# Performance work log

Measured on AMD Instinct MI355X. Metric: run time of the kernel, lower is better.

Reference implementation:

```python
import jax, jax.numpy as jnp
import numpy as np

B, D_IN = 4096, 1024
E, K = 16, 2
EMB = 256
H1, H2 = 2048, 1024  # hidden_units, hidden_units // 2
O = 512              # num_classes


def setup_inputs() -> dict:
    key = jax.random.key(0)
    ks = jax.random.split(key, 10)
    s = lambda *sh: 1.0 / np.sqrt(sh[-2] if len(sh) > 1 else 1.0)
    return {
        "x":   jax.random.normal(ks[0], (B, D_IN), jnp.float32),
        "Wr":  jax.random.normal(ks[1], (D_IN, EMB), jnp.float32) * (1.0 / np.sqrt(D_IN)),
        "br":  jnp.zeros((EMB,), jnp.float32),
        "emb": jax.random.normal(ks[2], (E, EMB), jnp.float32) * (1.0 / np.sqrt(EMB)),
        "W1":  jax.random.normal(ks[3], (E, D_IN, H1), jnp.float32) * (1.0 / np.sqrt(D_IN)),
        "b1":  jnp.zeros((E, H1), jnp.float32),
        "W2":  jax.random.normal(ks[4], (E, H1, H2), jnp.float32) * (1.0 / np.sqrt(H1)),
        "b2":  jnp.zeros((E, H2), jnp.float32),
        "W3":  jax.random.normal(ks[5], (E, H2, O), jnp.float32) * (1.0 / np.sqrt(H2)),
        "b3":  jnp.zeros((E, O), jnp.float32),
    }


def reference(x, Wr, br, emb, W1, b1, W2, b2, W3, b3):
    # Router query: [B, EMB]
    q = x @ Wr + br
    # Negative squared euclidean distance to expert embeddings -> scores [B, E]
    d2 = jnp.sum(jnp.square(q[:, None, :] - emb[None, :, :]), axis=-1)
    scores = -d2
    gating_probs = jax.nn.softmax(scores, axis=-1)  # [B, E]
    # Top-k selection + renormalized gates
    top_v, top_i = jax.lax.top_k(scores, K)          # [B, K]
    gates = jax.nn.softmax(top_v, axis=-1)           # [B, K]
    # All experts run on full batch (dense), batched over expert axis
    h1 = jax.nn.relu(jnp.einsum('bi,eih->beh', x, W1) + b1)   # [B, E, H1]
    h2 = jax.nn.relu(jnp.einsum('beh,ehm->bem', h1, W2) + b2)  # [B, E, H2]
    out = jnp.einsum('bem,emo->beo', h2, W3) + b3              # [B, E, O]
    # Gather top-k expert outputs per example and combine
    sel = jnp.take_along_axis(out, top_i[:, :, None], axis=1)  # [B, K, O]
    final = jnp.sum(sel * gates[:, :, None], axis=1)           # [B, O]
    return final, q, gating_probs
```

## Files before the change

### kernel.cpp

```cpp
#include <hip/hip_runtime.h>
#include <hip/hip_bf16.h>

using bf16 = __hip_bfloat16;
typedef __attribute__((ext_vector_type(8))) short bf16x8;
typedef __attribute__((ext_vector_type(8))) unsigned short u16x8;
typedef __attribute__((ext_vector_type(4))) float f32x4;

constexpr int BATCH = 4096;
constexpr int D_IN  = 1024;
constexpr int NEXP  = 16;
constexpr int EMB   = 256;
constexpr int H1    = 2048;
constexpr int H2    = 1024;
constexpr int OUTD  = 512;
constexpr int SLOTS = BATCH * 2;
constexpr int SLOTS_PAD = SLOTS + 256;
constexpr int MAX_T256 = SLOTS / 256 + NEXP;
constexpr int MAX_T128 = SLOTS / 128 + NEXP;
constexpr int K3    = 3 * D_IN;

constexpr size_t WS_XB     = 0;
constexpr size_t WS_XLO    = WS_XB     + (size_t)BATCH * D_IN * 2;
constexpr size_t WS_H1     = WS_XLO    + (size_t)BATCH * D_IN * 2;
constexpr size_t WS_H2     = WS_H1     + (size_t)SLOTS_PAD * H1 * 2;
constexpr size_t WS_OSL    = WS_H2     + (size_t)SLOTS_PAD * H2 * 2;
constexpr size_t WS_TOPI   = WS_OSL    + (size_t)SLOTS_PAD * OUTD * 4;
constexpr size_t WS_GATES  = WS_TOPI   + (size_t)SLOTS * 4;
constexpr size_t WS_SLOTOF = WS_GATES  + (size_t)SLOTS * 4;
constexpr size_t WS_TOKL   = WS_SLOTOF + (size_t)SLOTS * 4;
constexpr size_t WS_CNT    = WS_TOKL   + (size_t)SLOTS_PAD * 4;
constexpr size_t WS_TMAP256= WS_CNT    + 64 * 4;
constexpr size_t WS_TMAP128= WS_TMAP256+ (size_t)MAX_T256 * 8;
constexpr size_t WS_WR3    = ((WS_TMAP128 + (size_t)MAX_T128 * 8) + 255) & ~(size_t)255;
constexpr size_t WS_WT     = ((WS_WR3 + (size_t)EMB * K3 * 2) + 255) & ~(size_t)255;

__device__ __forceinline__ unsigned short f2bf(float f) {
    bf16 h = __float2bfloat16(f);
    return __builtin_bit_cast(unsigned short, h);
}
__device__ __forceinline__ float bf2f(unsigned short h) {
    return __builtin_bit_cast(float, (unsigned)h << 16);
}

__device__ __forceinline__ void gload16(const unsigned short* g, unsigned short* l) {
    __builtin_amdgcn_global_load_lds(
        (const __attribute__((address_space(1))) unsigned int*)g,
        (__attribute__((address_space(3))) unsigned int*)l, 16, 0, 0);
}

template <int N>
__device__ __forceinline__ void waitcnt_vm() {
    static_assert(N == 0 || N == 4 || N == 8, "add case");
    if constexpr (N == 0) asm volatile("s_waitcnt vmcnt(0)" ::: "memory");
    else if constexpr (N == 4) asm volatile("s_waitcnt vmcnt(4)" ::: "memory");
    else if constexpr (N == 8) asm volatile("s_waitcnt vmcnt(8)" ::: "memory");
}

__global__ __launch_bounds__(256) void k_cvt_x(const float* __restrict__ x,
                                               unsigned short* __restrict__ xhi,
                                               unsigned short* __restrict__ xlo) {
    int i = blockIdx.x * 256 + threadIdx.x;
    float4 v = reinterpret_cast<const float4*>(x)[i];
    ushort4 h, l;
    h.x = f2bf(v.x); h.y = f2bf(v.y); h.z = f2bf(v.z); h.w = f2bf(v.w);
    l.x = f2bf(v.x - bf2f(h.x)); l.y = f2bf(v.y - bf2f(h.y));
    l.z = f2bf(v.z - bf2f(h.z)); l.w = f2bf(v.w - bf2f(h.w));
    reinterpret_cast<ushort4*>(xhi)[i] = h;
    reinterpret_cast<ushort4*>(xlo)[i] = l;
}

__global__ __launch_bounds__(256) void k_wr3(const float* __restrict__ Wr,
                                             unsigned short* __restrict__ Wrt3) {
    __shared__ float Tf[64][65];
    int n0 = blockIdx.x * 64, k0 = blockIdx.y * 64;
    const float* Wb = Wr + (size_t)k0 * EMB + n0;
    int t  = threadIdx.x;
    int kr = t >> 4, c4 = (t & 15) * 4;
#pragma unroll
    for (int i = 0; i < 4; i++) {
        float4 v = *reinterpret_cast<const float4*>(Wb + (size_t)(kr + i * 16) * EMB + c4);
        Tf[kr + i * 16][c4 + 0] = v.x; Tf[kr + i * 16][c4 + 1] = v.y;
        Tf[kr + i * 16][c4 + 2] = v.z; Tf[kr + i * 16][c4 + 3] = v.w;
    }
    __syncthreads();
#pragma unroll
    for (int i = 0; i < 2; i++) {
        int idx = t + i * 256;
        int n = idx >> 3, ck = (idx & 7) * 8;
        u16x8 hi, lo;
#pragma unroll
        for (int j = 0; j < 8; j++) {
            float w = Tf[ck + j][n];
            unsigned short h = f2bf(w);
            hi[j] = h; lo[j] = f2bf(w - bf2f(h));
        }
        unsigned short* dst = Wrt3 + (size_t)(n0 + n) * K3 + k0 + ck;
        *reinterpret_cast<u16x8*>(dst)            = hi;
        *reinterpret_cast<u16x8*>(dst + D_IN)     = hi;
        *reinterpret_cast<u16x8*>(dst + 2 * D_IN) = lo;
    }
}

__global__ __launch_bounds__(256) void k_wtrans(const float* __restrict__ W,
                                                unsigned short* __restrict__ Wt,
                                                int KD, int ND) {
    __shared__ float Tf[64][65];
    int e = blockIdx.z;
    int n0 = blockIdx.x * 64, k0 = blockIdx.y * 64;
    const float* Wb = W + ((size_t)e * KD + k0) * ND + n0;
    int t  = threadIdx.x;
    int kr = t >> 4, c4 = (t & 15) * 4;
#pragma unroll
    for (int i = 0; i < 4; i++) {
        float4 v = *reinterpret_cast<const float4*>(Wb + (size_t)(kr + i * 16) * ND + c4);
        Tf[kr + i * 16][c4 + 0] = v.x; Tf[kr + i * 16][c4 + 1] = v.y;
        Tf[kr + i * 16][c4 + 2] = v.z; Tf[kr + i * 16][c4 + 3] = v.w;
    }
    __syncthreads();
    unsigned short* Wtb = Wt + ((size_t)e * ND + n0) * KD + k0;
#pragma unroll
    for (int i = 0; i < 2; i++) {
        int idx = t + i * 256;
        int n = idx >> 3, ck = (idx & 7) * 8;
        u16x8 o;
#pragma unroll
        for (int j = 0; j < 8; j++) o[j] = f2bf(Tf[ck + j][n]);
        *reinterpret_cast<u16x8*>(Wtb + (size_t)n * KD + ck) = o;
    }
}

__global__ __launch_bounds__(256) void k_router3(const unsigned short* __restrict__ xhi,
                                                 const unsigned short* __restrict__ xlo,
                                                 const unsigned short* __restrict__ wrt3,
                                                 const float* __restrict__ br,
                                                 float* __restrict__ qout) {
    int nb = blockIdx.x * 64;
    int mb = blockIdx.y * 64;

    __shared__ __align__(16) unsigned short As[2][64 * 64];
    __shared__ __align__(16) unsigned short Bs[2][64 * 64];

    int t    = threadIdx.x;
    int lane = t & 63;
    int w    = t >> 6;
    int wr   = (w >> 1) * 32;
    int wc   = (w & 1) * 32;

    int srow = t >> 3;
    int swz  = (t & 7) ^ (srow & 7);
    size_t aoff[2], boff[2];
#pragma unroll
    for (int i = 0; i < 2; i++) {
        int row = i * 32 + srow;
        aoff[i] = (size_t)(mb + row) * D_IN + swz * 8;
        boff[i] = (size_t)(nb + row) * K3 + swz * 8;
    }

    auto STAGE = [&](int buf, int tts) {
        const unsigned short* abase = (tts >= 16 && tts < 32) ? xlo : xhi;
        int kk = (tts & 15) * 64;
#pragma unroll
        for (int i = 0; i < 2; i++) {
            gload16(abase + aoff[i] + kk, &As[buf][(i * 32 + w * 8) * 64] + lane * 8);
            gload16(wrt3 + boff[i] + tts * 64, &Bs[buf][(i * 32 + w * 8) * 64] + lane * 8);
        }
    };

    f32x4 acc[2][2];
#pragma unroll
    for (int mi = 0; mi < 2; mi++)
#pragma unroll
        for (int ni = 0; ni < 2; ni++) acc[mi][ni] = {0.f, 0.f, 0.f, 0.f};

    int lr  = lane & 15;
    int lkc = lane >> 4;

    constexpr int NT = K3 / 64;
    STAGE(0, 0);
    STAGE(1, 1);

    for (int tt = 0; tt < NT; tt++) {
        int cur = tt & 1;
        if (tt + 1 < NT) waitcnt_vm<4>(); else waitcnt_vm<0>();
        __builtin_amdgcn_s_barrier();
        const char* Ab = (const char*)As[cur];
        const char* Bb = (const char*)Bs[cur];
#pragma unroll
        for (int ks = 0; ks < 2; ks++) {
            bf16x8 a[2], b[2];
#pragma unroll
            for (int mi = 0; mi < 2; mi++) {
                int row = wr + mi * 16 + lr;
                int c   = (lkc + ks * 4) ^ (row & 7);
                a[mi] = *reinterpret_cast<const bf16x8*>(Ab + row * 128 + c * 16);
            }
#pragma unroll
            for (int ni = 0; ni < 2; ni++) {
                int row = wc + ni * 16 + lr;
                int c   = (lkc + ks * 4) ^ (row & 7);
                b[ni] = *reinterpret_cast<const bf16x8*>(Bb + row * 128 + c * 16);
            }
#pragma unroll
            for (int mi = 0; mi < 2; mi++)
#pragma unroll
                for (int ni = 0; ni < 2; ni++)
                    acc[mi][ni] = __builtin_amdgcn_mfma_f32_16x16x32_bf16(a[mi], b[ni], acc[mi][ni], 0, 0, 0);
        }
        __builtin_amdgcn_s_barrier();
        if (tt + 2 < NT) STAGE(cur, tt + 2);
    }

    int rowbase = (lane >> 4) * 4;
#pragma unroll
    for (int ni = 0; ni < 2; ni++) {
        int col = nb + wc + ni * 16 + lr;
        float bv = br[col];
#pragma unroll
        for (int mi = 0; mi < 2; mi++) {
#pragma unroll
            for (int qi = 0; qi < 4; qi++) {
                int row = mb + wr + mi * 16 + rowbase + qi;
                qout[(size_t)row * EMB + col] = acc[mi][ni][qi] + bv;
            }
        }
    }
}

__global__ __launch_bounds__(256) void k_router_topk(const float* __restrict__ q,
                                                     const float* __restrict__ emb,
                                                     float* __restrict__ gp,
                                                     int* __restrict__ topi,
                                                     float* __restrict__ gates) {
    int b    = blockIdx.x * 4 + (threadIdx.x >> 6);
    int lane = threadIdx.x & 63;
    int e    = lane & 15;
    int seg  = (lane >> 4) * 64;
    const float* qr = q + (size_t)b * EMB + seg;
    const float* er = emb + (size_t)e * EMB + seg;
    float d2 = 0.f;
#pragma unroll 8
    for (int i = 0; i < 64; i++) { float d = qr[i] - er[i]; d2 = fmaf(d, d, d2); }
    d2 += __shfl_xor(d2, 16);
    d2 += __shfl_xor(d2, 32);
    float s = -d2;
    float m = s;
#pragma unroll
    for (int o = 1; o < 16; o <<= 1) m = fmaxf(m, __shfl_xor(m, o));
    float ex  = __expf(s - m);
    float sum = ex;
#pragma unroll
    for (int o = 1; o < 16; o <<= 1) sum += __shfl_xor(sum, o);
    if (lane < 16) gp[(size_t)b * NEXP + lane] = ex / sum;
    float v1 = s; int i1 = e;
#pragma unroll
    for (int o = 1; o < 16; o <<= 1) {
        float ov = __shfl_xor(v1, o); int oi = __shfl_xor(i1, o);
        if (ov > v1 || (ov == v1 && oi < i1)) { v1 = ov; i1 = oi; }
    }
    float s2 = (e == i1) ? -1e30f : s;
    float v2 = s2; int i2 = e;
#pragma unroll
    for (int o = 1; o < 16; o <<= 1) {
        float ov = __shfl_xor(v2, o); int oi = __shfl_xor(i2, o);
        if (ov > v2 || (ov == v2 && oi < i2)) { v2 = ov; i2 = oi; }
    }
    if (lane == 0) {
        topi[b * 2] = i1; topi[b * 2 + 1] = i2;
        float tv  = __expf(v2 - v1);
        float inv = 1.f / (1.f + tv);
        gates[b * 2] = inv; gates[b * 2 + 1] = tv * inv;
    }
}

__global__ void k_zero(int* counts) { if (threadIdx.x < NEXP) counts[threadIdx.x] = 0; }

__global__ __launch_bounds__(256) void k_count(const int* __restrict__ topi, int* __restrict__ counts) {
    int i = blockIdx.x * 256 + threadIdx.x;
    atomicAdd(&counts[topi[i]], 1);
}

__global__ void k_scan(const int* __restrict__ counts, int* __restrict__ offsets,
                       int* __restrict__ cursors, int2* __restrict__ tmap256,
                       int2* __restrict__ tmap128) {
    if (threadIdx.x != 0) return;
    int off = 0;
    for (int e = 0; e < NEXP; e++) {
        offsets[e] = off; cursors[e] = off;
        off += counts[e];
    }
    for (int i = 0; i < MAX_T256; i++) tmap256[i] = make_int2(-1, 0);
    for (int i = 0; i < MAX_T128; i++) tmap128[i] = make_int2(-1, 0);
    {
        int binload[8] = {0, 0, 0, 0, 0, 0, 0, 0};
        for (int e = 0; e < NEXP; e++) {
            int rem = (counts[e] + 255) >> 8, ti = 0;
            while (rem > 0) {
                int b = 0;
                for (int q2 = 1; q2 < 8; q2++)
                    if (binload[q2] < binload[b]) b = q2;
                int space = 6 - binload[b];
                if (space <= 0) break;
                int take = (rem < space) ? rem : space;
                for (int i = 0; i < take; i++)
                    tmap256[b * 6 + binload[b] + i] = make_int2(e, (ti + i) * 256);
                binload[b] += take; ti += take; rem -= take;
            }
        }
    }
    {
        int binload[8] = {0, 0, 0, 0, 0, 0, 0, 0};
        for (int e = 0; e < NEXP; e++) {
            int rem = (counts[e] + 127) >> 7, ti = 0;
            while (rem > 0) {
                int b = 0;
                for (int q2 = 1; q2 < 8; q2++)
                    if (binload[q2] < binload[b]) b = q2;
                int space = 10 - binload[b];
                if (space <= 0) break;
                int take = (rem < space) ? rem : space;
                for (int i = 0; i < take; i++)
                    tmap128[b * 10 + binload[b] + i] = make_int2(e, (ti + i) * 128);
                binload[b] += take; ti += take; rem -= take;
            }
        }
    }
}

__global__ __launch_bounds__(256) void k_scatter(const int* __restrict__ topi, int* __restrict__ cursors,
                                                 int* __restrict__ toklist, int* __restrict__ slotof) {
    int i = blockIdx.x * 256 + threadIdx.x;
    int e = topi[i];
    int s = atomicAdd(&cursors[e], 1);
    toklist[s] = i >> 1;
    slotof[i]  = s;
}

template <int KD, int ND, int BM, int BN, int WM, int WN, int MODE, int MINW, int CAP>
__global__ __launch_bounds__(WM * WN * 64, MINW) void k_gemm(
    const unsigned short* __restrict__ Xin, const unsigned short* __restrict__ Wt,
    const float* __restrict__ bg, unsigned short* __restrict__ Hout,
    float* __restrict__ Oout, const int* __restrict__ counts,
    const int* __restrict__ offsets, const int* __restrict__ toklist,
    const int2* __restrict__ tmap) {
    constexpr int THREADS = WM * WN * 64;
    constexpr int FM = BM / (WM * 16);
    constexpr int FN = BN / (WN * 16);
    constexpr int A_ISS = BM * 8 / THREADS;
    constexpr int B_ISS = BN * 8 / THREADS;
    constexpr int RPI = THREADS / 8;
    constexpr int SL  = A_ISS + B_ISS;

    int id  = blockIdx.x;
    int bin = id & 7;
    int j   = id >> 3;
    int y   = bin * CAP + j % CAP;
    int xnb = j / CAP;

    int2 tm = tmap[y];
    int e = tm.x;
    if (e < 0) return;
    int base = tm.y;
    int n_e  = counts[e];
    int off  = offsets[e];
    int n0   = xnb * BN;

    __shared__ __align__(16) unsigned short As[2][BM * 64];
    __shared__ __align__(16) unsigned short Bs[2][BN * 64];

    int t    = threadIdx.x;
    int lane = t & 63;
    int w    = t >> 6;
    int wm   = w / WN;
    int wn   = w % WN;

    int srow  = t >> 3;
    int chunk = t & 7;
    const unsigned short* asrc[A_ISS];
    const unsigned short* bsrc[B_ISS];
#pragma unroll
    for (int i = 0; i < A_ISS; i++) {
        int row = i * RPI + srow;
        int swz = chunk ^ (row & 7);
        int g   = base + row;
        size_t arow;
        if (MODE == 0) {
            int gg = (g < n_e) ? g : (n_e - 1);
            arow = (size_t)toklist[off + gg];
        } else {
            arow = (size_t)(off + g);
        }
        asrc[i] = Xin + arow * KD + swz * 8;
    }
#pragma unroll
    for (int i = 0; i < B_ISS; i++) {
        int row = i * RPI + srow;
        int swz = chunk ^ (row & 7);
        bsrc[i] = Wt + ((size_t)e * ND + n0 + row) * KD + swz * 8;
    }

    auto STAGE = [&](int buf, int kt) {
#pragma unroll
        for (int i = 0; i < A_ISS; i++)
            gload16(asrc[i] + kt, &As[buf][(i * RPI + w * 8) * 64] + lane * 8);
#pragma unroll
        for (int i = 0; i < B_ISS; i++)
            gload16(bsrc[i] + kt, &Bs[buf][(i * RPI + w * 8) * 64] + lane * 8);
    };

    f32x4 acc[FM][FN];
#pragma unroll
    for (int mi = 0; mi < FM; mi++)
#pragma unroll
        for (int ni = 0; ni < FN; ni++) acc[mi][ni] = {0.f, 0.f, 0.f, 0.f};

    int lr  = lane & 15;
    int lkc = lane >> 4;

    constexpr int NT = KD / 64;
    STAGE(0, 0);
    STAGE(1, 64);

    for (int tt = 0; tt < NT; tt++) {
        int cur = tt & 1;
        if (tt + 1 < NT) waitcnt_vm<SL>(); else waitcnt_vm<0>();
        __builtin_amdgcn_s_barrier();
        const char* Ab = (const char*)As[cur];
        const char* Bb = (const char*)Bs[cur];
#pragma unroll
        for (int ks = 0; ks < 2; ks++) {
            bf16x8 b[FN];
#pragma unroll
            for (int ni = 0; ni < FN; ni++) {
                int row = wn * (BN / WN) + ni * 16 + lr;
                int c   = (lkc + ks * 4) ^ (row & 7);
                b[ni] = *reinterpret_cast<const bf16x8*>(Bb + row * 128 + c * 16);
            }
            bf16x8 a[FM];
#pragma unroll
            for (int mi = 0; mi < FM; mi++) {
                int row = wm * (BM / WM) + mi * 16 + lr;
                int c   = (lkc + ks * 4) ^ (row & 7);
                a[mi] = *reinterpret_cast<const bf16x8*>(Ab + row * 128 + c * 16);
            }
#pragma unroll
            for (int mi = 0; mi < FM; mi++)
#pragma unroll
                for (int ni = 0; ni < FN; ni++)
                    acc[mi][ni] = __builtin_amdgcn_mfma_f32_16x16x32_bf16(a[mi], b[ni], acc[mi][ni], 0, 0, 0);
        }
        __builtin_amdgcn_s_barrier();
        if (tt + 2 < NT) STAGE(cur, (tt + 2) * 64);
    }

    int rowbase = (lane >> 4) * 4;
#pragma unroll
    for (int ni = 0; ni < FN; ni++) {
        int col = n0 + wn * (BN / WN) + ni * 16 + lr;
        float bv = bg[(size_t)e * ND + col];
#pragma unroll
        for (int mi = 0; mi < FM; mi++) {
#pragma unroll
            for (int qi = 0; qi < 4; qi++) {
                int g = base + wm * (BM / WM) + mi * 16 + rowbase + qi;
                if (g < n_e) {
                    float v = acc[mi][ni][qi] + bv;
                    if (MODE == 2) {
                        Oout[(size_t)(off + g) * ND + col] = v;
                    } else {
                        v = fmaxf(v, 0.f);
                        Hout[(size_t)(off + g) * ND + col] = f2bf(v);
                    }
                }
            }
        }
    }
}

__global__ __launch_bounds__(128) void k_combine(const float* __restrict__ osl,
                                                 const float* __restrict__ gates,
                                                 const int* __restrict__ slotof,
                                                 float* __restrict__ outf) {
    int b = blockIdx.x;
    int j = threadIdx.x;
    int s0 = slotof[b * 2], s1 = slotof[b * 2 + 1];
    float g0 = gates[b * 2], g1 = gates[b * 2 + 1];
    float4 o0 = reinterpret_cast<const float4*>(osl + (size_t)s0 * OUTD)[j];
    float4 o1 = reinterpret_cast<const float4*>(osl + (size_t)s1 * OUTD)[j];
    float4 r;
    r.x = g0 * o0.x + g1 * o1.x;
    r.y = g0 * o0.y + g1 * o1.y;
    r.z = g0 * o0.z + g1 * o1.z;
    r.w = g0 * o0.w + g1 * o1.w;
    reinterpret_cast<float4*>(outf + (size_t)b * OUTD)[j] = r;
}

extern "C" void kernel_launch(void* const* d_in, const int* in_sizes, int n_in,
                              void* d_out, int out_size, void* d_ws, size_t ws_size,
                              hipStream_t stream) {
    const float* x   = (const float*)d_in[0];
    const float* Wr  = (const float*)d_in[1];
    const float* br  = (const float*)d_in[2];
    const float* emb = (const float*)d_in[3];
    const float* W1  = (const float*)d_in[4];
    const float* b1  = (const float*)d_in[5];
    const float* W2  = (const float*)d_in[6];
    const float* b2  = (const float*)d_in[7];
    const float* W3  = (const float*)d_in[8];
    const float* b3  = (const float*)d_in[9];

    float* out_final = (float*)d_out;
    float* out_q     = out_final + (size_t)BATCH * OUTD;
    float* out_gp    = out_q + (size_t)BATCH * EMB;

    char* ws = (char*)d_ws;
    unsigned short* xb  = (unsigned short*)(ws + WS_XB);
    unsigned short* xlo = (unsigned short*)(ws + WS_XLO);
    unsigned short* h1  = (unsigned short*)(ws + WS_H1);
    unsigned short* h2  = (unsigned short*)(ws + WS_H2);
    float* osl    = (float*)(ws + WS_OSL);
    int*   topi   = (int*)(ws + WS_TOPI);
    float* gates  = (float*)(ws + WS_GATES);
    int*   slotof = (int*)(ws + WS_SLOTOF);
    int*   toklist= (int*)(ws + WS_TOKL);
    int*   counts = (int*)(ws + WS_CNT);
    int*   offsets= counts + 16;
    int*   cursors= counts + 32;
    int2*  tmap256= (int2*)(ws + WS_TMAP256);
    int2*  tmap128= (int2*)(ws + WS_TMAP128);
    unsigned short* wrt3 = (unsigned short*)(ws + WS_WR3);
    unsigned short* wt   = (unsigned short*)(ws + WS_WT);

    k_cvt_x<<<BATCH * D_IN / 4 / 256, 256, 0, stream>>>(x, xb, xlo);
    k_wr3<<<dim3(EMB / 64, D_IN / 64), 256, 0, stream>>>(Wr, wrt3);
    k_router3<<<dim3(EMB / 64, BATCH / 64), 256, 0, stream>>>(xb, xlo, wrt3, br, out_q);
    k_router_topk<<<BATCH / 4, 256, 0, stream>>>(out_q, emb, out_gp, topi, gates);
    k_zero<<<1, 64, 0, stream>>>(counts);
    k_count<<<SLOTS / 256, 256, 0, stream>>>(topi, counts);
    k_scan<<<1, 64, 0, stream>>>(counts, offsets, cursors, tmap256, tmap128);
    k_scatter<<<SLOTS / 256, 256, 0, stream>>>(topi, cursors, toklist, slotof);

    k_wtrans<<<dim3(H1 / 64, D_IN / 64, NEXP), 256, 0, stream>>>(W1, wt, D_IN, H1);
    k_gemm<D_IN, H1, 256, 256, 2, 4, 0, 1, 6><<<(H1 / 256) * 48, 512, 0, stream>>>(
        xb, wt, b1, h1, nullptr, counts, offsets, toklist, tmap256);

    k_wtrans<<<dim3(H2 / 64, H1 / 64, NEXP), 256, 0, stream>>>(W2, wt, H1, H2);
    k_gemm<H1, H2, 256, 256, 2, 4, 1, 1, 6><<<(H2 / 256) * 48, 512, 0, stream>>>(
        h1, wt, b2, h2, nullptr, counts, offsets, toklist, tmap256);

    k_wtrans<<<dim3(OUTD / 64, H2 / 64, NEXP), 256, 0, stream>>>(W3, wt, H2, OUTD);
    k_gemm<H2, OUTD, 128, 128, 2, 2, 2, 2, 10><<<(OUTD / 128) * 80, 256, 0, stream>>>(
        h2, wt, b3, nullptr, osl, counts, offsets, toklist, tmap128);

    k_combine<<<BATCH, 128, 0, stream>>>(osl, gates, slotof, out_final);
}
```

Baseline: 385.4 us.

## Merge prep kernels and fold W1/W2 transposes into router launch

Fuses x conversion, router-weight packing and count zeroing into one launch, and folds the expert-count atomics into the top-k kernel. When the workspace is large enough, it also runs the W1 and W2 transposes as extra blocks of the router GEMM launch, writing into two separate buffers so they run alongside the small router GEMM. This cuts kernel launches and lets the transpose traffic overlap router work. The cost is a larger workspace, extra branches and shared memory sized to the largest role.

Measured after the change: 453.0 us. +17.5%, slower.

```diff
diff --git a/kernel.cpp b/kernel.cpp
--- a/kernel.cpp
+++ b/kernel.cpp
@@ -33,6 +33,9 @@
 constexpr size_t WS_TMAP128= WS_TMAP256+ (size_t)MAX_T256 * 8;
 constexpr size_t WS_WR3    = ((WS_TMAP128 + (size_t)MAX_T128 * 8) + 255) & ~(size_t)255;
 constexpr size_t WS_WT     = ((WS_WR3 + (size_t)EMB * K3 * 2) + 255) & ~(size_t)255;
+constexpr size_t WT_BYTES  = (size_t)NEXP * H1 * D_IN * 2;
+constexpr size_t WS_WTB    = WS_WT + WT_BYTES;
+constexpr size_t NEED2     = WS_WTB + WT_BYTES;
 
 __device__ __forceinline__ unsigned short f2bf(float f) {
     bf16 h = __float2bfloat16(f);
@@ -56,65 +59,19 @@
     else if constexpr (N == 8) asm volatile("s_waitcnt vmcnt(8)" ::: "memory");
 }
 
-__global__ __launch_bounds__(256) void k_cvt_x(const float* __restrict__ x,
-                                               unsigned short* __restrict__ xhi,
-                                               unsigned short* __restrict__ xlo) {
-    int i = blockIdx.x * 256 + threadIdx.x;
-    float4 v = reinterpret_cast<const float4*>(x)[i];
-    ushort4 h, l;
-    h.x = f2bf(v.x); h.y = f2bf(v.y); h.z = f2bf(v.z); h.w = f2bf(v.w);
-    l.x = f2bf(v.x - bf2f(h.x)); l.y = f2bf(v.y - bf2f(h.y));
-    l.z = f2bf(v.z - bf2f(h.z)); l.w = f2bf(v.w - bf2f(h.w));
-    reinterpret_cast<ushort4*>(xhi)[i] = h;
-    reinterpret_cast<ushort4*>(xlo)[i] = l;
-}
-
-__global__ __launch_bounds__(256) void k_wr3(const float* __restrict__ Wr,
-                                             unsigned short* __restrict__ Wrt3) {
-    __shared__ float Tf[64][65];
-    int n0 = blockIdx.x * 64, k0 = blockIdx.y * 64;
-    const float* Wb = Wr + (size_t)k0 * EMB + n0;
+__device__ __forceinline__ void wtrans_body(const float* __restrict__ W,
+                                            unsigned short* __restrict__ Wt,
+                                            int KD, int ND, int e, int k0, int n0,
+                                            char* smem) {
+    float* Tf = (float*)smem;
     int t  = threadIdx.x;
     int kr = t >> 4, c4 = (t & 15) * 4;
-#pragma unroll
-    for (int i = 0; i < 4; i++) {
-        float4 v = *reinterpret_cast<const float4*>(Wb + (size_t)(kr + i * 16) * EMB + c4);
-        Tf[kr + i * 16][c4 + 0] = v.x; Tf[kr + i * 16][c4 + 1] = v.y;
-        Tf[kr + i * 16][c4 + 2] = v.z; Tf[kr + i * 16][c4 + 3] = v.w;
-    }
-    __syncthreads();
-#pragma unroll
-    for (int i = 0; i < 2; i++) {
-        int idx = t + i * 256;
-        int n = idx >> 3, ck = (idx & 7) * 8;
-        u16x8 hi, lo;
-#pragma unroll
-        for (int j = 0; j < 8; j++) {
-            float w = Tf[ck + j][n];
-            unsigned short h = f2bf(w);
-            hi[j] = h; lo[j] = f2bf(w - bf2f(h));
-        }
-        unsigned short* dst = Wrt3 + (size_t)(n0 + n) * K3 + k0 + ck;
-        *reinterpret_cast<u16x8*>(dst)            = hi;
-        *reinterpret_cast<u16x8*>(dst + D_IN)     = hi;
-        *reinterpret_cast<u16x8*>(dst + 2 * D_IN) = lo;
-    }
-}
-
-__global__ __launch_bounds__(256) void k_wtrans(const float* __restrict__ W,
-                                                unsigned short* __restrict__ Wt,
-                                                int KD, int ND) {
-    __shared__ float Tf[64][65];
-    int e = blockIdx.z;
-    int n0 = blockIdx.x * 64, k0 = blockIdx.y * 64;
     const float* Wb = W + ((size_t)e * KD + k0) * ND + n0;
-    int t  = threadIdx.x;
-    int kr = t >> 4, c4 = (t & 15) * 4;
 #pragma unroll
     for (int i = 0; i < 4; i++) {
         float4 v = *reinterpret_cast<const float4*>(Wb + (size_t)(kr + i * 16) * ND + c4);
-        Tf[kr + i * 16][c4 + 0] = v.x; Tf[kr + i * 16][c4 + 1] = v.y;
-        Tf[kr + i * 16][c4 + 2] = v.z; Tf[kr + i * 16][c4 + 3] = v.w;
+        Tf[(kr + i * 16) * 65 + c4 + 0] = v.x; Tf[(kr + i * 16) * 65 + c4 + 1] = v.y;
+        Tf[(kr + i * 16) * 65 + c4 + 2] = v.z; Tf[(kr + i * 16) * 65 + c4 + 3] = v.w;
     }
     __syncthreads();
     unsigned short* Wtb = Wt + ((size_t)e * ND + n0) * KD + k0;
@@ -124,21 +81,88 @@
         int n = idx >> 3, ck = (idx & 7) * 8;
         u16x8 o;
 #pragma unroll
-        for (int j = 0; j < 8; j++) o[j] = f2bf(Tf[ck + j][n]);
+        for (int j = 0; j < 8; j++) o[j] = f2bf(Tf[(ck + j) * 65 + n]);
         *reinterpret_cast<u16x8*>(Wtb + (size_t)n * KD + ck) = o;
     }
 }
 
-__global__ __launch_bounds__(256) void k_router3(const unsigned short* __restrict__ xhi,
-                                                 const unsigned short* __restrict__ xlo,
-                                                 const unsigned short* __restrict__ wrt3,
-                                                 const float* __restrict__ br,
-                                                 float* __restrict__ qout) {
-    int nb = blockIdx.x * 64;
-    int mb = blockIdx.y * 64;
-
-    __shared__ __align__(16) unsigned short As[2][64 * 64];
-    __shared__ __align__(16) unsigned short Bs[2][64 * 64];
+__global__ __launch_bounds__(256) void k_prep(const float* __restrict__ x,
+                                              unsigned short* __restrict__ xhi,
+                                              unsigned short* __restrict__ xlo,
+                                              const float* __restrict__ Wr,
+                                              unsigned short* __restrict__ Wrt3,
+                                              int* __restrict__ counts) {
+    __shared__ float Tf[64][65];
+    int bx = blockIdx.x, t = threadIdx.x;
+    if (bx < 4096) {
+        int i = bx * 256 + t;
+        float4 v = reinterpret_cast<const float4*>(x)[i];
+        ushort4 h, l;
+        h.x = f2bf(v.x); h.y = f2bf(v.y); h.z = f2bf(v.z); h.w = f2bf(v.w);
+        l.x = f2bf(v.x - bf2f(h.x)); l.y = f2bf(v.y - bf2f(h.y));
+        l.z = f2bf(v.z - bf2f(h.z)); l.w = f2bf(v.w - bf2f(h.w));
+        reinterpret_cast<ushort4*>(xhi)[i] = h;
+        reinterpret_cast<ushort4*>(xlo)[i] = l;
+    } else if (bx < 4160) {
+        int idx = bx - 4096;
+        int n0 = (idx & 3) * 64, k0 = (idx >> 2) * 64;
+        const float* Wb = Wr + (size_t)k0 * EMB + n0;
+        int kr = t >> 4, c4 = (t & 15) * 4;
+#pragma unroll
+        for (int i = 0; i < 4; i++) {
+            float4 v = *reinterpret_cast<const float4*>(Wb + (size_t)(kr + i * 16) * EMB + c4);
+            Tf[kr + i * 16][c4 + 0] = v.x; Tf[kr + i * 16][c4 + 1] = v.y;
+            Tf[kr + i * 16][c4 + 2] = v.z; Tf[kr + i * 16][c4 + 3] = v.w;
+        }
+        __syncthreads();
+#pragma unroll
+        for (int i = 0; i < 2; i++) {
+            int idx2 = t + i * 256;
+            int n = idx2 >> 3, ck = (idx2 & 7) * 8;
+            u16x8 hi, lo;
+#pragma unroll
+            for (int j = 0; j < 8; j++) {
+                float w = Tf[ck + j][n];
+                unsigned short h = f2bf(w);
+                hi[j] = h; lo[j] = f2bf(w - bf2f(h));
+            }
+            unsigned short* dst = Wrt3 + (size_t)(n0 + n) * K3 + k0 + ck;
+            *reinterpret_cast<u16x8*>(dst)            = hi;
+            *reinterpret_cast<u16x8*>(dst + D_IN)     = hi;
+            *reinterpret_cast<u16x8*>(dst + 2 * D_IN) = lo;
+        }
+    } else {
+        if (t < 16) counts[t] = 0;
+    }
+}
+
+__global__ __launch_bounds__(256) void k_router_wt(const unsigned short* __restrict__ xhi,
+                                                   const unsigned short* __restrict__ xlo,
+                                                   const unsigned short* __restrict__ wrt3,
+                                                   const float* __restrict__ br,
+                                                   float* __restrict__ qout,
+                                                   const float* __restrict__ W1,
+                                                   unsigned short* __restrict__ wt1,
+                                                   const float* __restrict__ W2,
+                                                   unsigned short* __restrict__ wt2) {
+    __shared__ __align__(16) char smem[32768];
+    int bx = blockIdx.x;
+    if (bx >= 256) {
+        int idx = bx - 256;
+        if (idx < 8192) {
+            int e = idx >> 9, rem = idx & 511;
+            wtrans_body(W1, wt1, D_IN, H1, e, (rem >> 5) << 6, (rem & 31) << 6, smem);
+        } else {
+            int i2 = idx - 8192;
+            int e = i2 >> 9, rem = i2 & 511;
+            wtrans_body(W2, wt2, H1, H2, e, (rem >> 4) << 6, (rem & 15) << 6, smem);
+        }
+        return;
+    }
+    unsigned short* As = (unsigned short*)smem;
+    unsigned short* Bs = As + 8192;
+    int nb = (bx & 3) * 64;
+    int mb = (bx >> 2) * 64;
 
     int t    = threadIdx.x;
     int lane = t & 63;
@@ -161,8 +185,8 @@
         int kk = (tts & 15) * 64;
 #pragma unroll
         for (int i = 0; i < 2; i++) {
-            gload16(abase + aoff[i] + kk, &As[buf][(i * 32 + w * 8) * 64] + lane * 8);
-            gload16(wrt3 + boff[i] + tts * 64, &Bs[buf][(i * 32 + w * 8) * 64] + lane * 8);
+            gload16(abase + aoff[i] + kk, As + buf * 4096 + (i * 32 + w * 8) * 64 + lane * 8);
+            gload16(wrt3 + boff[i] + tts * 64, Bs + buf * 4096 + (i * 32 + w * 8) * 64 + lane * 8);
         }
     };
 
@@ -183,8 +207,8 @@
         int cur = tt & 1;
         if (tt + 1 < NT) waitcnt_vm<4>(); else waitcnt_vm<0>();
         __builtin_amdgcn_s_barrier();
-        const char* Ab = (const char*)As[cur];
-        const char* Bb = (const char*)Bs[cur];
+        const char* Ab = (const char*)(As + cur * 4096);
+        const char* Bb = (const char*)(Bs + cur * 4096);
 #pragma unroll
         for (int ks = 0; ks < 2; ks++) {
             bf16x8 a[2], b[2];
@@ -226,11 +250,12 @@
     }
 }
 
-__global__ __launch_bounds__(256) void k_router_topk(const float* __restrict__ q,
-                                                     const float* __restrict__ emb,
-                                                     float* __restrict__ gp,
-                                                     int* __restrict__ topi,
-                                                     float* __restrict__ gates) {
+__global__ __launch_bounds__(256) void k_topk_count(const float* __restrict__ q,
+                                                    const float* __restrict__ emb,
+                                                    float* __restrict__ gp,
+                                                    int* __restrict__ topi,
+                                                    float* __restrict__ gates,
+                                                    int* __restrict__ counts) {
     int b    = blockIdx.x * 4 + (threadIdx.x >> 6);
     int lane = threadIdx.x & 63;
     int e    = lane & 15;
@@ -269,14 +294,9 @@
         float tv  = __expf(v2 - v1);
         float inv = 1.f / (1.f + tv);
         gates[b * 2] = inv; gates[b * 2 + 1] = tv * inv;
-    }
-}
-
-__global__ void k_zero(int* counts) { if (threadIdx.x < NEXP) counts[threadIdx.x] = 0; }
-
-__global__ __launch_bounds__(256) void k_count(const int* __restrict__ topi, int* __restrict__ counts) {
-    int i = blockIdx.x * 256 + threadIdx.x;
-    atomicAdd(&counts[topi[i]], 1);
+        atomicAdd(&counts[i1], 1);
+        atomicAdd(&counts[i2], 1);
+    }
 }
 
 __global__ void k_scan(const int* __restrict__ counts, int* __restrict__ offsets,
@@ -335,6 +355,13 @@
     slotof[i]  = s;
 }
 
+__global__ __launch_bounds__(256) void k_wtrans(const float* __restrict__ W,
+                                                unsigned short* __restrict__ Wt,
+                                                int KD, int ND) {
+    __shared__ __align__(16) char smem[64 * 65 * 4];
+    wtrans_body(W, Wt, KD, ND, blockIdx.z, blockIdx.y * 64, blockIdx.x * 64, smem);
+}
+
 template <int KD, int ND, int BM, int BN, int WM, int WN, int MODE, int MINW, int CAP>
 __global__ __launch_bounds__(WM * WN * 64, MINW) void k_gemm(
     const unsigned short* __restrict__ Xin, const unsigned short* __restrict__ Wt,
@@ -528,28 +555,36 @@
     int2*  tmap256= (int2*)(ws + WS_TMAP256);
     int2*  tmap128= (int2*)(ws + WS_TMAP128);
     unsigned short* wrt3 = (unsigned short*)(ws + WS_WR3);
-    unsigned short* wt   = (unsigned short*)(ws + WS_WT);
-
-    k_cvt_x<<<BATCH * D_IN / 4 / 256, 256, 0, stream>>>(x, xb, xlo);
-    k_wr3<<<dim3(EMB / 64, D_IN / 64), 256, 0, stream>>>(Wr, wrt3);
-    k_router3<<<dim3(EMB / 64, BATCH / 64), 256, 0, stream>>>(xb, xlo, wrt3, br, out_q);
-    k_router_topk<<<BATCH / 4, 256, 0, stream>>>(out_q, emb, out_gp, topi, gates);
-    k_zero<<<1, 64, 0, stream>>>(counts);
-    k_count<<<SLOTS / 256, 256, 0, stream>>>(topi, counts);
+    unsigned short* wtA  = (unsigned short*)(ws + WS_WT);
+    unsigned short* wtB  = (unsigned short*)(ws + WS_WTB);
+
+    const bool t2 = (ws_size >= NEED2);
+
+    k_prep<<<4161, 256, 0, stream>>>(x, xb, xlo, Wr, wrt3, counts);
+
+    if (t2) {
+        k_router_wt<<<256 + 8192 + 8192, 256, 0, stream>>>(
+            xb, xlo, wrt3, br, out_q, W1, wtA, W2, wtB);
+    } else {
+        k_router_wt<<<256, 256, 0, stream>>>(
+            xb, xlo, wrt3, br, out_q, nullptr, nullptr, nullptr, nullptr);
+    }
+
+    k_topk_count<<<BATCH / 4, 256, 0, stream>>>(out_q, emb, out_gp, topi, gates, counts);
     k_scan<<<1, 64, 0, stream>>>(counts, offsets, cursors, tmap256, tmap128);
     k_scatter<<<SLOTS / 256, 256, 0, stream>>>(topi, cursors, toklist, slotof);
 
-    k_wtrans<<<dim3(H1 / 64, D_IN / 64, NEXP), 256, 0, stream>>>(W1, wt, D_IN, H1);
+    if (!t2) k_wtrans<<<dim3(H1 / 64, D_IN / 64, NEXP), 256, 0, stream>>>(W1, wtA, D_IN, H1);
     k_gemm<D_IN, H1, 256, 256, 2, 4, 0, 1, 6><<<(H1 / 256) * 48, 512, 0, stream>>>(
-        xb, wt, b1, h1, nullptr, counts, offsets, toklist, tmap256);
-
-    k_wtrans<<<dim3(H2 / 64, H1 / 64, NEXP), 256, 0, stream>>>(W2, wt, H1, H2);
+        xb, wtA, b1, h1, nullptr, counts, offsets, toklist, tmap256);
+
+    if (!t2) k_wtrans<<<dim3(H2 / 64, H1 / 64, NEXP), 256, 0, stream>>>(W2, wtA, H1, H2);
     k_gemm<H1, H2, 256, 256, 2, 4, 1, 1, 6><<<(H2 / 256) * 48, 512, 0, stream>>>(
-        h1, wt, b2, h2, nullptr, counts, offsets, toklist, tmap256);
-
-    k_wtrans<<<dim3(OUTD / 64, H2 / 64, NEXP), 256, 0, stream>>>(W3, wt, H2, OUTD);
+        h1, t2 ? wtB : wtA, b2, h2, nullptr, counts, offsets, toklist, tmap256);
+
+    k_wtrans<<<dim3(OUTD / 64, H2 / 64, NEXP), 256, 0, stream>>>(W3, wtA, H2, OUTD);
     k_gemm<H2, OUTD, 128, 128, 2, 2, 2, 2, 10><<<(OUTD / 128) * 80, 256, 0, stream>>>(
-        h2, wt, b3, nullptr, osl, counts, offsets, toklist, tmap128);
+        h2, wtA, b3, nullptr, osl, counts, offsets, toklist, tmap128);
 
     k_combine<<<BATCH, 128, 0, stream>>>(osl, gates, slotof, out_final);
 }
```
